# Kernel tuning notes

Hardware: AMD Instinct MI355X
Metric: run time of the kernel (lower is better)

Reference implementation:

```python
import jax, jax.numpy as jnp
import numpy as np


def setup_inputs() -> dict:
    key = jax.random.key(0)
    ks = jax.random.split(key, 7)
    B, C, H, W = 16, 256, 1, 4096
    x = jax.random.normal(ks[0], (B, C, H, W), dtype=jnp.float32)
    init = lambda k, s: jax.random.normal(k, s, dtype=jnp.float32) * 0.02
    return {
        "x": x,
        "Wq": init(ks[1], (C, C)), "bq": jnp.zeros((C,), jnp.float32),
        "Wk": init(ks[2], (C, C)), "bk": jnp.zeros((C,), jnp.float32),
        "Wv": init(ks[3], (C, C)), "bv": jnp.zeros((C,), jnp.float32),
    }


def reference(x, Wq, bq, Wk, bk, Wv, bv):
    B, C, H, W = x.shape
    xs = jnp.transpose(x[:, :, 0, :], (0, 2, 1))  # [B, W, C]
    Q = xs @ Wq.T + bq  # [B, W, C]
    K = xs @ Wk.T + bk
    V = xs @ Wv.T + bv
    scale = jnp.sqrt(jnp.asarray(C, dtype=Q.dtype))

    # radius-1 sliding window along width; pad so window gather is static
    Kp = jnp.pad(K, ((0, 0), (1, 1), (0, 0)))  # [B, W+2, C]
    Vp = jnp.pad(V, ((0, 0), (1, 1), (0, 0)))
    idx = jnp.arange(W)[:, None] + jnp.arange(3)[None, :]  # padded indices [W,3]
    pos = idx - 1  # original positions (may be -1 or W -> invalid at edges)
    valid = (pos >= 0) & (pos < W)  # [W, 3]

    Kw = Kp[:, idx]  # [B, W, 3, C]
    Vw = Vp[:, idx]  # [B, W, 3, C]

    scores = jnp.einsum('bwc,bwkc->bwk', Q, Kw) / scale  # [B, W, 3]
    scores = jnp.where(valid[None], scores, jnp.asarray(-1e9, scores.dtype))
    attn = jax.nn.softmax(scores, axis=-1)
    out = jnp.einsum('bwk,bwkc->bwc', attn, Vw)  # [B, W, C]
    # [B, W, C] -> [B, C, 1, W]
    return jnp.transpose(out, (0, 2, 1))[:, :, None, :]
```

## Files before the change

### kernel.cpp

```cpp
#include <hip/hip_runtime.h>
#include <hip/hip_bf16.h>

#define C_DIM 256
#define W_DIM 4096
#define LDS_BYTES 162512

typedef unsigned short u16;
typedef short s16x8 __attribute__((ext_vector_type(8)));
typedef unsigned short u16x8 __attribute__((ext_vector_type(8)));
typedef unsigned short u16x4 __attribute__((ext_vector_type(4)));
typedef float f32x16 __attribute__((ext_vector_type(16)));

__device__ __forceinline__ u16 f2b(float f) {
  return __builtin_bit_cast(u16, __float2bfloat16(f));
}
__device__ __forceinline__ float b2f(u16 u) {
  return __builtin_bit_cast(float, ((unsigned)u) << 16);
}

__global__ __launch_bounds__(256) void prep_kernel(
    const float* __restrict__ Wq, const float* __restrict__ bq,
    const float* __restrict__ Wk, const float* __restrict__ bk,
    const float* __restrict__ Wv, char* __restrict__ ws) {
  u16* Mb   = (u16*)ws;
  u16* Wvb  = (u16*)(ws + 131072);
  float* u0 = (float*)(ws + 262144);
  float* u1 = (float*)(ws + 263168);
  float* c0p = (float*)(ws + 264192);
  int bid = blockIdx.x, t = threadIdx.x;
  if (bid < 256) {
    __shared__ float Wqs[256*17];
    __shared__ float Wks[256*17];
    int i0 = (bid >> 4) << 4, j0 = (bid & 15) << 4;
    for (int it = 0; it < 16; ++it) {
      int e = t + 256*it; int a = e >> 4, ii = e & 15;
      Wqs[a*17+ii] = Wq[a*256 + i0 + ii];
      Wks[a*17+ii] = Wk[a*256 + j0 + ii];
    }
    __syncthreads();
    int ii = t >> 4, jj = t & 15;
    float acc = 0.f;
    #pragma unroll 8
    for (int a = 0; a < 256; ++a) acc += Wqs[a*17+ii] * Wks[a*17+jj];
    Mb[(i0+ii)*256 + j0 + jj] = f2b(acc);
  } else if (bid == 256) {
    int j = t;
    float a0 = 0.f, a1 = 0.f;
    #pragma unroll 4
    for (int a = 0; a < 256; ++a) {
      a0 += bq[a] * Wk[a*256 + j];
      a1 += bk[a] * Wq[a*256 + j];
    }
    u0[j] = a0; u1[j] = a1;
    __shared__ float red[256];
    red[t] = bq[t] * bk[t];
    __syncthreads();
    if (t == 0) { float s = 0.f; for (int a = 0; a < 256; ++a) s += red[a]; *c0p = s; }
  } else {
    int base = ((bid - 257)*256 + t) * 4;
    const float4 v = *reinterpret_cast<const float4*>(Wv + base);
    ushort4 pk = make_ushort4(f2b(v.x), f2b(v.y), f2b(v.z), f2b(v.w));
    *reinterpret_cast<ushort4*>(Wvb + base) = pk;
  }
}

__global__ __launch_bounds__(512, 2) void main_kernel(
    const float* __restrict__ x, const char* __restrict__ ws,
    const float* __restrict__ bv, float* __restrict__ out) {
  const u16* Mb   = (const u16*)ws;
  const u16* Wvb  = (const u16*)(ws + 131072);
  const float* u0g = (const float*)(ws + 262144);
  const float* u1g = (const float*)(ws + 263168);
  const float c0  = *(const float*)(ws + 264192);

  extern __shared__ char lds[];
  u16*   Xt  = (u16*)lds;
  float* Ps  = (float*)(lds + 132608);
  float* ABs = (float*)(lds + 157376);
  float* U   = (float*)(lds + 159440);
  float* bvs = (float*)(lds + 161488);

  const int bid = blockIdx.x;
  const int t = threadIdx.x;
  const int wv = t >> 6, l = t & 63;
  const int col = l & 31, half = l >> 5;

  const int b  = bid >> 4;
  const int cw = bid & 15;
  const int w0 = cw << 8;
  const float* xb = x + (size_t)b * (C_DIM*W_DIM);
  float* outb = out + (size_t)b * (C_DIM*W_DIM);

  if (t < 256) { U[t] = u0g[t]; U[256+t] = u1g[t]; bvs[t] = bv[t]; }
  __syncthreads();

  {
    #pragma unroll
    for (int p = 0; p < 4; ++p) {
      int j = 64*p + l;
      int w = w0 - 1 + j;
      bool ok = (w >= 0);
      const float* xp = xb + w;
      float xr[32];
      #pragma unroll
      for (int g = 0; g < 4; ++g)
        #pragma unroll
        for (int e = 0; e < 8; ++e)
          xr[g*8+e] = ok ? xp[(size_t)((4*wv+g)*8 + e) * W_DIM] : 0.f;
      float pa = 0.f, pb_ = 0.f;
      #pragma unroll
      for (int g = 0; g < 4; ++g) {
        int kk = 4*wv + g;
        union { u16 u[8]; u16x8 v; } pk;
        #pragma unroll
        for (int e = 0; e < 8; ++e) {
          float v = xr[g*8+e];
          pk.u[e] = f2b(v);
          pa  += U[kk*8+e] * v;
          pb_ += U[256 + kk*8+e] * v;
        }
        *reinterpret_cast<u16x8*>(Xt + (kk*259 + j)*8) = pk.v;
      }
      Ps[wv*258 + j] = pa;
      Ps[2064 + wv*258 + j] = pb_;
    }
    if (l < 3) {
      int j = 256 + l;
      int w = w0 - 1 + j;
      bool real = (l < 2) && (w < W_DIM);
      const float* xpe = xb + w;
      float pa = 0.f, pb_ = 0.f;
      #pragma unroll
      for (int g = 0; g < 4; ++g) {
        int kk = 4*wv + g;
        union { u16 u[8]; u16x8 v; } pk;
        #pragma unroll
        for (int e = 0; e < 8; ++e) {
          float v = real ? xpe[(size_t)(kk*8+e) * W_DIM] : 0.f;
          pk.u[e] = f2b(v);
          pa  += U[kk*8+e] * v;
          pb_ += U[256 + kk*8+e] * v;
        }
        *reinterpret_cast<u16x8*>(Xt + (kk*259 + j)*8) = pk.v;
      }
      if (l < 2) {
        Ps[wv*258 + j] = pa;
        Ps[2064 + wv*258 + j] = pb_;
      }
    }
  }
  __syncthreads();

  f32x16 acc[9];
  #pragma unroll
  for (int n = 0; n < 9; ++n)
    #pragma unroll
    for (int r = 0; r < 16; ++r) acc[n][r] = 0.f;
  {
    int j8 = 256 + col; if (j8 > 258) j8 = 258;
    const u16* Arow = Mb + (32*wv + col)*256 + 8*half;
    #pragma unroll
    for (int kk = 0; kk < 16; ++kk) {
      s16x8 a = *reinterpret_cast<const s16x8*>(Arow + 16*kk);
      const u16* Bb = Xt + (2*kk + half)*259*8;
      #pragma unroll
      for (int n = 0; n < 8; ++n) {
        s16x8 bfr = *reinterpret_cast<const s16x8*>(Bb + (32*n + col)*8);
        acc[n] = __builtin_amdgcn_mfma_f32_32x32x16_bf16(a, bfr, acc[n], 0, 0, 0);
      }
      s16x8 bfr8 = *reinterpret_cast<const s16x8*>(Bb + j8*8);
      acc[8] = __builtin_amdgcn_mfma_f32_32x32x16_bf16(a, bfr8, acc[8], 0, 0, 0);
    }
  }
  for (int i = t; i < 516; i += 512) {
    int which = (i >= 258) ? 1 : 0;
    int jj = i - 258*which;
    float s = 0.f;
    #pragma unroll
    for (int g = 0; g < 8; ++g) s += Ps[which*2064 + g*258 + jj];
    ABs[which*258 + jj] = s;
  }
  __syncthreads();

  {
    #pragma unroll
    for (int n = 0; n < 9; ++n) {
      int jt = (n < 8) ? (32*n + col) : (256 + col);
      int jm = jt - 1; if (jm < 0) jm = 0; if (jm > 258) jm = 258;
      int jc = (jt > 258) ? 258 : jt;
      int jp_ = jt + 1; if (jp_ > 258) jp_ = 258;
      float s0 = 0.f, s1 = 0.f, s2 = 0.f;
      #pragma unroll
      for (int q = 0; q < 4; ++q) {
        const u16* base = Xt + (4*wv + q)*259*8 + 4*half;
        u16x4 xm = *reinterpret_cast<const u16x4*>(base + jm*8);
        u16x4 xc = *reinterpret_cast<const u16x4*>(base + jc*8);
        u16x4 xp = *reinterpret_cast<const u16x4*>(base + jp_*8);
        #pragma unroll
        for (int r4 = 0; r4 < 4; ++r4) {
          float g0 = acc[n][4*q + r4];
          s2 += g0 * b2f(xm[r4]);
          s1 += g0 * b2f(xc[r4]);
          s0 += g0 * b2f(xp[r4]);
        }
      }
      s0 += __shfl_xor(s0, 32);
      s1 += __shfl_xor(s1, 32);
      s2 += __shfl_xor(s2, 32);
      if (half == 0) {
        if (jt <= 255)             Ps[0*2064 + wv*258 + jt+1] = s0;
        if (jt >= 1 && jt <= 256)  Ps[1*2064 + wv*258 + jt]   = s1;
        if (jt >= 2 && jt <= 257)  Ps[2*2064 + wv*258 + jt-1] = s2;
      }
    }
  }
  __syncthreads();

  {
    float aw0[4], aw1[4], aw2[4];
    #pragma unroll
    for (int p = 0; p < 4; ++p) {
      int oc = 64*p + l;
      int jp = oc + 1;
      float d0 = 0.f, d1 = 0.f, d2 = 0.f;
      #pragma unroll
      for (int g = 0; g < 8; ++g) {
        d0 += Ps[0*2064 + g*258 + jp];
        d1 += Ps[1*2064 + g*258 + jp];
        d2 += Ps[2*2064 + g*258 + jp];
      }
      float am = ABs[jp-1], ac_ = ABs[jp], ap_ = ABs[jp+1];
      float be = ABs[258 + jp];
      float sc0 = (d0 + am + be + c0) * 0.0625f;
      float sc1 = (d1 + ac_ + be + c0) * 0.0625f;
      float sc2 = (d2 + ap_ + be + c0) * 0.0625f;
      int w = w0 + oc;
      bool v0 = (w >= 1), v2 = (w + 1 < W_DIM);
      const float NEG = -1e30f;
      float m = fmaxf(v0 ? sc0 : NEG, fmaxf(sc1, v2 ? sc2 : NEG));
      float e0v = v0 ? __expf(sc0 - m) : 0.f;
      float e1v = __expf(sc1 - m);
      float e2v = v2 ? __expf(sc2 - m) : 0.f;
      float inv = 1.f / (e0v + e1v + e2v);
      aw0[p] = e0v*inv; aw1[p] = e1v*inv; aw2[p] = e2v*inv;
    }
    #pragma unroll
    for (int g = 0; g < 4; ++g) {
      u16* base = Xt + (4*wv + g)*259*8;
      u16x8 xrd[12];
      #pragma unroll
      for (int p = 0; p < 4; ++p)
        #pragma unroll
        for (int i = 0; i < 3; ++i)
          xrd[p*3+i] = *reinterpret_cast<const u16x8*>(base + (64*p + l + i)*8);
      __builtin_amdgcn_sched_barrier(0);
      #pragma unroll
      for (int p = 0; p < 4; ++p) {
        union { u16 u[8]; u16x8 v; } pk;
        #pragma unroll
        for (int e = 0; e < 8; ++e)
          pk.u[e] = f2b(aw0[p]*b2f(xrd[p*3][e]) + aw1[p]*b2f(xrd[p*3+1][e])
                        + aw2[p]*b2f(xrd[p*3+2][e]));
        *reinterpret_cast<u16x8*>(base + (64*p + l + 1)*8) = pk.v;
      }
      __builtin_amdgcn_sched_barrier(0);
    }
  }
  __syncthreads();

  {
    f32x16 acc2[8];
    #pragma unroll
    for (int n = 0; n < 8; ++n)
      #pragma unroll
      for (int r = 0; r < 16; ++r) acc2[n][r] = 0.f;
    const u16* Arow2 = Wvb + (32*wv + col)*256 + 8*half;
    #pragma unroll
    for (int kk = 0; kk < 16; ++kk) {
      s16x8 a = *reinterpret_cast<const s16x8*>(Arow2 + 16*kk);
      const u16* Bb = Xt + (2*kk + half)*259*8;
      #pragma unroll
      for (int n = 0; n < 8; ++n) {
        s16x8 bfr = *reinterpret_cast<const s16x8*>(Bb + (1 + 32*n + col)*8);
        acc2[n] = __builtin_amdgcn_mfma_f32_32x32x16_bf16(a, bfr, acc2[n], 0, 0, 0);
      }
    }
    float bvr[16];
    #pragma unroll
    for (int q = 0; q < 4; ++q) {
      const float4 t4 = *reinterpret_cast<const float4*>(bvs + 32*wv + 8*q + 4*half);
      bvr[4*q+0] = t4.x; bvr[4*q+1] = t4.y; bvr[4*q+2] = t4.z; bvr[4*q+3] = t4.w;
    }
    #pragma unroll
    for (int n = 0; n < 8; ++n)
      #pragma unroll
      for (int r = 0; r < 16; ++r) {
        int crow = 32*wv + (r&3) + 8*(r>>2) + 4*half;
        outb[(size_t)crow*W_DIM + w0 + 32*n + col] = acc2[n][r] + bvr[r];
      }
  }
}

extern "C" void kernel_launch(void* const* d_in, const int* in_sizes, int n_in,
                              void* d_out, int out_size, void* d_ws, size_t ws_size,
                              hipStream_t stream) {
  (void)in_sizes; (void)n_in; (void)out_size; (void)ws_size;
  const float* x  = (const float*)d_in[0];
  const float* Wq = (const float*)d_in[1];
  const float* bq = (const float*)d_in[2];
  const float* Wk = (const float*)d_in[3];
  const float* bk = (const float*)d_in[4];
  const float* Wv = (const float*)d_in[5];
  const float* bv = (const float*)d_in[6];
  float* out = (float*)d_out;
  char* ws = (char*)d_ws;

  hipFuncSetAttribute((const void*)main_kernel,
                      hipFuncAttributeMaxDynamicSharedMemorySize, LDS_BYTES);
  prep_kernel<<<321, 256, 0, stream>>>(Wq, bq, Wk, bk, Wv, ws);
  main_kernel<<<256, 512, LDS_BYTES, stream>>>(x, ws, bv, out);
}
```

Baseline: 78.39 us.

## Double block to 1024 threads, splitting MFMA column tiles across wave halves

The main kernel now launches 1024 threads per block instead of 512. Each 32-row group of waves handles half the 32-column output tiles, and the x-load and prep phase is split across twice as many waves, with partial dot products merged through LDS atomicAdd. The ninth edge MFMA tile is replaced by a small scalar dot-product pass whose results are written into a few shared slots for the last window positions. The goal is more waves in flight and lower register pressure per wave, at the cost of LDS atomics, an extra zeroing pass, and the same occupancy limit, since LDS use still allows only one block per CU.

```diff
diff --git a/kernel.cpp b/kernel.cpp
--- a/kernel.cpp
+++ b/kernel.cpp
@@ -3,7 +3,7 @@
 
 #define C_DIM 256
 #define W_DIM 4096
-#define LDS_BYTES 162512
+#define LDS_BYTES 162528
 
 typedef unsigned short u16;
 typedef short s16x8 __attribute__((ext_vector_type(8)));
@@ -64,7 +64,7 @@
   }
 }
 
-__global__ __launch_bounds__(512, 2) void main_kernel(
+__global__ __launch_bounds__(1024, 4) void main_kernel(
     const float* __restrict__ x, const char* __restrict__ ws,
     const float* __restrict__ bv, float* __restrict__ out) {
   const u16* Mb   = (const u16*)ws;
@@ -77,13 +77,17 @@
   u16*   Xt  = (u16*)lds;
   float* Ps  = (float*)(lds + 132608);
   float* ABs = (float*)(lds + 157376);
-  float* U   = (float*)(lds + 159440);
-  float* bvs = (float*)(lds + 161488);
+  float* fS  = (float*)(lds + 159440);
+  float* U   = (float*)(lds + 159456);
+  float* bvs = (float*)(lds + 161504);
 
   const int bid = blockIdx.x;
   const int t = threadIdx.x;
   const int wv = t >> 6, l = t & 63;
   const int col = l & 31, half = l >> 5;
+  const int rg = wv & 7, nh = wv >> 3;
+  const int nbase = 4*nh;
+  const int kkA = 2*wv;
 
   const int b  = bid >> 4;
   const int cw = bid & 15;
@@ -91,6 +95,8 @@
   const float* xb = x + (size_t)b * (C_DIM*W_DIM);
   float* outb = out + (size_t)b * (C_DIM*W_DIM);
 
+  for (int i = t; i < 6192; i += 1024) Ps[i] = 0.f;
+  if (t < 4) fS[t] = 0.f;
   if (t < 256) { U[t] = u0g[t]; U[256+t] = u1g[t]; bvs[t] = bv[t]; }
   __syncthreads();
 
@@ -101,28 +107,29 @@
       int w = w0 - 1 + j;
       bool ok = (w >= 0);
       const float* xp = xb + w;
-      float xr[32];
-      #pragma unroll
-      for (int g = 0; g < 4; ++g)
+      float xr[16];
+      #pragma unroll
+      for (int g2 = 0; g2 < 2; ++g2)
         #pragma unroll
         for (int e = 0; e < 8; ++e)
-          xr[g*8+e] = ok ? xp[(size_t)((4*wv+g)*8 + e) * W_DIM] : 0.f;
+          xr[g2*8+e] = ok ? xp[(size_t)((kkA+g2)*8 + e) * W_DIM] : 0.f;
       float pa = 0.f, pb_ = 0.f;
       #pragma unroll
-      for (int g = 0; g < 4; ++g) {
-        int kk = 4*wv + g;
+      for (int g2 = 0; g2 < 2; ++g2) {
+        int kk = kkA + g2;
         union { u16 u[8]; u16x8 v; } pk;
         #pragma unroll
         for (int e = 0; e < 8; ++e) {
-          float v = xr[g*8+e];
+          float v = xr[g2*8+e];
           pk.u[e] = f2b(v);
-          pa  += U[kk*8+e] * v;
-          pb_ += U[256 + kk*8+e] * v;
+          int c = kk*8 + e;
+          pa  += U[c] * v;
+          pb_ += U[256 + c] * v;
         }
         *reinterpret_cast<u16x8*>(Xt + (kk*259 + j)*8) = pk.v;
       }
-      Ps[wv*258 + j] = pa;
-      Ps[2064 + wv*258 + j] = pb_;
+      atomicAdd(&Ps[rg*258 + j], pa);
+      atomicAdd(&Ps[2064 + rg*258 + j], pb_);
     }
     if (l < 3) {
       int j = 256 + l;
@@ -131,48 +138,73 @@
       const float* xpe = xb + w;
       float pa = 0.f, pb_ = 0.f;
       #pragma unroll
-      for (int g = 0; g < 4; ++g) {
-        int kk = 4*wv + g;
+      for (int g2 = 0; g2 < 2; ++g2) {
+        int kk = kkA + g2;
         union { u16 u[8]; u16x8 v; } pk;
         #pragma unroll
         for (int e = 0; e < 8; ++e) {
           float v = real ? xpe[(size_t)(kk*8+e) * W_DIM] : 0.f;
           pk.u[e] = f2b(v);
-          pa  += U[kk*8+e] * v;
-          pb_ += U[256 + kk*8+e] * v;
+          int c = kk*8 + e;
+          pa  += U[c] * v;
+          pb_ += U[256 + c] * v;
         }
         *reinterpret_cast<u16x8*>(Xt + (kk*259 + j)*8) = pk.v;
       }
       if (l < 2) {
-        Ps[wv*258 + j] = pa;
-        Ps[2064 + wv*258 + j] = pb_;
-      }
-    }
-  }
-  __syncthreads();
-
-  f32x16 acc[9];
+        atomicAdd(&Ps[rg*258 + j], pa);
+        atomicAdd(&Ps[2064 + rg*258 + j], pb_);
+      }
+    }
+  }
+  __syncthreads();
+
+  f32x16 acc[4];
   #pragma unroll
-  for (int n = 0; n < 9; ++n)
-    #pragma unroll
-    for (int r = 0; r < 16; ++r) acc[n][r] = 0.f;
-  {
-    int j8 = 256 + col; if (j8 > 258) j8 = 258;
-    const u16* Arow = Mb + (32*wv + col)*256 + 8*half;
+  for (int ni = 0; ni < 4; ++ni)
+    #pragma unroll
+    for (int r = 0; r < 16; ++r) acc[ni][r] = 0.f;
+  {
+    const u16* Arow = Mb + (32*rg + col)*256 + 8*half;
     #pragma unroll
     for (int kk = 0; kk < 16; ++kk) {
       s16x8 a = *reinterpret_cast<const s16x8*>(Arow + 16*kk);
       const u16* Bb = Xt + (2*kk + half)*259*8;
       #pragma unroll
-      for (int n = 0; n < 8; ++n) {
-        s16x8 bfr = *reinterpret_cast<const s16x8*>(Bb + (32*n + col)*8);
-        acc[n] = __builtin_amdgcn_mfma_f32_32x32x16_bf16(a, bfr, acc[n], 0, 0, 0);
-      }
-      s16x8 bfr8 = *reinterpret_cast<const s16x8*>(Bb + j8*8);
-      acc[8] = __builtin_amdgcn_mfma_f32_32x32x16_bf16(a, bfr8, acc[8], 0, 0, 0);
-    }
-  }
-  for (int i = t; i < 516; i += 512) {
+      for (int ni = 0; ni < 4; ++ni) {
+        s16x8 bfr = *reinterpret_cast<const s16x8*>(Bb + (32*(nbase+ni) + col)*8);
+        acc[ni] = __builtin_amdgcn_mfma_f32_32x32x16_bf16(a, bfr, acc[ni], 0, 0, 0);
+      }
+    }
+  }
+
+  {
+    int i = t >> 2, kq = t & 3;
+    float xi255 = b2f(Xt[((i>>3)*259 + 255)*8 + (i&7)]);
+    float xi256 = b2f(Xt[((i>>3)*259 + 256)*8 + (i&7)]);
+    float a1 = 0.f, a2 = 0.f;
+    const u16* Mrow = Mb + i*256 + 64*kq;
+    #pragma unroll
+    for (int kk8 = 0; kk8 < 8; ++kk8) {
+      int sA = 8*kq + kk8;
+      s16x8 m8 = *reinterpret_cast<const s16x8*>(Mrow + 8*kk8);
+      u16x8 xk6 = *reinterpret_cast<const u16x8*>(Xt + (sA*259 + 256)*8);
+      u16x8 xk7 = *reinterpret_cast<const u16x8*>(Xt + (sA*259 + 257)*8);
+      #pragma unroll
+      for (int e = 0; e < 8; ++e) {
+        float m = b2f((u16)m8[e]);
+        a1 += m * b2f(xk6[e]);
+        a2 += m * b2f(xk7[e]);
+      }
+    }
+    float p1 = xi256*a1, p2 = xi256*a2, p3 = xi255*a1;
+    #pragma unroll
+    for (int d = 1; d < 64; d <<= 1) {
+      p1 += __shfl_xor(p1, d); p2 += __shfl_xor(p2, d); p3 += __shfl_xor(p3, d);
+    }
+    if (l == 0) { atomicAdd(&fS[0], p1); atomicAdd(&fS[1], p2); atomicAdd(&fS[2], p3); }
+  }
+  for (int i = t; i < 516; i += 1024) {
     int which = (i >= 258) ? 1 : 0;
     int jj = i - 258*which;
     float s = 0.f;
@@ -184,21 +216,20 @@
 
   {
     #pragma unroll
-    for (int n = 0; n < 9; ++n) {
-      int jt = (n < 8) ? (32*n + col) : (256 + col);
-      int jm = jt - 1; if (jm < 0) jm = 0; if (jm > 258) jm = 258;
-      int jc = (jt > 258) ? 258 : jt;
-      int jp_ = jt + 1; if (jp_ > 258) jp_ = 258;
+    for (int ni = 0; ni < 4; ++ni) {
+      int jt = 32*(nbase+ni) + col;
+      int jm = (jt > 0) ? jt-1 : 0;
+      int jp = jt + 1;
       float s0 = 0.f, s1 = 0.f, s2 = 0.f;
       #pragma unroll
       for (int q = 0; q < 4; ++q) {
-        const u16* base = Xt + (4*wv + q)*259*8 + 4*half;
+        const u16* base = Xt + (4*rg + q)*259*8 + 4*half;
         u16x4 xm = *reinterpret_cast<const u16x4*>(base + jm*8);
-        u16x4 xc = *reinterpret_cast<const u16x4*>(base + jc*8);
-        u16x4 xp = *reinterpret_cast<const u16x4*>(base + jp_*8);
+        u16x4 xc = *reinterpret_cast<const u16x4*>(base + jt*8);
+        u16x4 xp = *reinterpret_cast<const u16x4*>(base + jp*8);
         #pragma unroll
         for (int r4 = 0; r4 < 4; ++r4) {
-          float g0 = acc[n][4*q + r4];
+          float g0 = acc[ni][4*q + r4];
           s2 += g0 * b2f(xm[r4]);
           s1 += g0 * b2f(xc[r4]);
           s0 += g0 * b2f(xp[r4]);
@@ -208,9 +239,9 @@
       s1 += __shfl_xor(s1, 32);
       s2 += __shfl_xor(s2, 32);
       if (half == 0) {
-        if (jt <= 255)             Ps[0*2064 + wv*258 + jt+1] = s0;
-        if (jt >= 1 && jt <= 256)  Ps[1*2064 + wv*258 + jt]   = s1;
-        if (jt >= 2 && jt <= 257)  Ps[2*2064 + wv*258 + jt-1] = s2;
+        Ps[0*2064 + rg*258 + jt+1] = s0;
+        if (jt >= 1) Ps[1*2064 + rg*258 + jt]   = s1;
+        if (jt >= 2) Ps[2*2064 + rg*258 + jt-1] = s2;
       }
     }
   }
@@ -229,6 +260,8 @@
         d1 += Ps[1*2064 + g*258 + jp];
         d2 += Ps[2*2064 + g*258 + jp];
       }
+      if (oc == 255)      { d1 = fS[0]; d2 = fS[1]; }
+      else if (oc == 254) { d2 = fS[2]; }
       float am = ABs[jp-1], ac_ = ABs[jp], ap_ = ABs[jp+1];
       float be = ABs[258 + jp];
       float sc0 = (d0 + am + be + c0) * 0.0625f;
@@ -245,8 +278,8 @@
       aw0[p] = e0v*inv; aw1[p] = e1v*inv; aw2[p] = e2v*inv;
     }
     #pragma unroll
-    for (int g = 0; g < 4; ++g) {
-      u16* base = Xt + (4*wv + g)*259*8;
+    for (int g2 = 0; g2 < 2; ++g2) {
+      u16* base = Xt + (kkA + g2)*259*8;
       u16x8 xrd[12];
       #pragma unroll
       for (int p = 0; p < 4; ++p)
@@ -269,34 +302,33 @@
   __syncthreads();
 
   {
-    f32x16 acc2[8];
-    #pragma unroll
-    for (int n = 0; n < 8; ++n)
-      #pragma unroll
-      for (int r = 0; r < 16; ++r) acc2[n][r] = 0.f;
-    const u16* Arow2 = Wvb + (32*wv + col)*256 + 8*half;
+    #pragma unroll
+    for (int ni = 0; ni < 4; ++ni)
+      #pragma unroll
+      for (int r = 0; r < 16; ++r) acc[ni][r] = 0.f;
+    const u16* Arow2 = Wvb + (32*rg + col)*256 + 8*half;
     #pragma unroll
     for (int kk = 0; kk < 16; ++kk) {
       s16x8 a = *reinterpret_cast<const s16x8*>(Arow2 + 16*kk);
       const u16* Bb = Xt + (2*kk + half)*259*8;
       #pragma unroll
-      for (int n = 0; n < 8; ++n) {
-        s16x8 bfr = *reinterpret_cast<const s16x8*>(Bb + (1 + 32*n + col)*8);
-        acc2[n] = __builtin_amdgcn_mfma_f32_32x32x16_bf16(a, bfr, acc2[n], 0, 0, 0);
+      for (int ni = 0; ni < 4; ++ni) {
+        s16x8 bfr = *reinterpret_cast<const s16x8*>(Bb + (1 + 32*(nbase+ni) + col)*8);
+        acc[ni] = __builtin_amdgcn_mfma_f32_32x32x16_bf16(a, bfr, acc[ni], 0, 0, 0);
       }
     }
     float bvr[16];
     #pragma unroll
     for (int q = 0; q < 4; ++q) {
-      const float4 t4 = *reinterpret_cast<const float4*>(bvs + 32*wv + 8*q + 4*half);
+      const float4 t4 = *reinterpret_cast<const float4*>(bvs + 32*rg + 8*q + 4*half);
       bvr[4*q+0] = t4.x; bvr[4*q+1] = t4.y; bvr[4*q+2] = t4.z; bvr[4*q+3] = t4.w;
     }
     #pragma unroll
-    for (int n = 0; n < 8; ++n)
+    for (int ni = 0; ni < 4; ++ni)
       #pragma unroll
       for (int r = 0; r < 16; ++r) {
-        int crow = 32*wv + (r&3) + 8*(r>>2) + 4*half;
-        outb[(size_t)crow*W_DIM + w0 + 32*n + col] = acc2[n][r] + bvr[r];
+        int crow = 32*rg + (r&3) + 8*(r>>2) + 4*half;
+        outb[(size_t)crow*W_DIM + w0 + 32*(nbase+ni) + col] = acc[ni][r] + bvr[r];
       }
   }
 }
@@ -318,5 +350,5 @@
   hipFuncSetAttribute((const void*)main_kernel,
                       hipFuncAttributeMaxDynamicSharedMemorySize, LDS_BYTES);
   prep_kernel<<<321, 256, 0, stream>>>(Wq, bq, Wk, bk, Wv, ws);
-  main_kernel<<<256, 512, LDS_BYTES, stream>>>(x, ws, bv, out);
-}
+  main_kernel<<<256, 1024, LDS_BYTES, stream>>>(x, ws, bv, out);
+}
```

After: 87.93 us. 12.2% more time.
